# Performance work log

Hardware: AMD Instinct MI355X
Metric: run time of the kernel (lower is better)

## Reference

```python
import jax, jax.numpy as jnp
import numpy as np

B, S, D = 4, 2048, 1024
H, DK, DV = 16, 64, 64


def setup_inputs() -> dict:
    key = jax.random.key(0)
    kx, kq, kk, kv, ko = jax.random.split(key, 5)
    scale = 0.02
    return {
        "x": jax.random.normal(kx, (B, S, D), dtype=jnp.float32),
        "Wq": jax.random.normal(kq, (H, D, DK), dtype=jnp.float32) * scale,
        "Wk": jax.random.normal(kk, (H, D, DK), dtype=jnp.float32) * scale,
        "Wv": jax.random.normal(kv, (H, D, DV), dtype=jnp.float32) * scale,
        "Wo": jax.random.normal(ko, (H * DV, D), dtype=jnp.float32) * scale,
    }


def reference(x, Wq, Wk, Wv, Wo):
    # Per-head projections, batched over heads with einsum (same math as
    # the original per-head Linear loop).
    q = jnp.einsum("bsd,hdk->bhsk", x, Wq)  # [B,H,S,DK]
    k = jnp.einsum("bsd,hdk->bhsk", x, Wk)  # [B,H,S,DK]
    v = jnp.einsum("bsd,hdv->bhsv", x, Wv)  # [B,H,S,DV]

    scores = jnp.einsum("bhqk,bhsk->bhqs", q, k) / jnp.sqrt(
        jnp.asarray(DK, dtype=x.dtype)
    )  # [B,H,S,S]
    # Causal mask: position q attends only to s <= q.
    causal = jnp.tril(jnp.ones((S, S), dtype=bool))
    scores = jnp.where(causal, scores, jnp.asarray(-1e9, dtype=scores.dtype))
    attn = jax.nn.softmax(scores, axis=-1)

    ctx = jnp.einsum("bhqs,bhsv->bhqv", attn, v)  # [B,H,S,DV]
    # Concat heads: [B,S,H*DV], then output projection (no bias).
    ctx = ctx.transpose(0, 2, 1, 3).reshape(B, S, H * DV)
    return ctx @ Wo  # [B,S,D]
```

## Files before the change

### kernel.cpp

```cpp
#include <hip/hip_runtime.h>
#include <hip/hip_bf16.h>

#define SB 2048
#define DM 1024
#define NH 16
#define HD 64
#define BB 4
#define MTOT (BB * SB)
#define NW (DM * DM)
#define QSCALE 0.1803368801111244f

typedef __attribute__((ext_vector_type(8))) short bf16x8;
typedef __attribute__((ext_vector_type(4))) short bf16x4;
typedef __attribute__((ext_vector_type(4))) float f32x4;
typedef __attribute__((ext_vector_type(8))) __fp16 f16x8;
typedef __attribute__((ext_vector_type(4))) __fp16 f16x4;
typedef __attribute__((ext_vector_type(2))) __fp16 f16x2;

__device__ __forceinline__ short f2bf(float f) {
    union { float f; unsigned u; } a; a.f = f;
    unsigned r = (a.u + 0x7FFF + ((a.u >> 16) & 1)) >> 16;
    return (short)r;
}

__global__ __launch_bounds__(256) void cvt_all(const float* __restrict__ x,
                                               const float* __restrict__ Wq,
                                               const float* __restrict__ Wk,
                                               const float* __restrict__ Wv,
                                               const float* __restrict__ Wo,
                                               short* __restrict__ xb,
                                               short* __restrict__ wall,
                                               short* __restrict__ wot) {
    const int bid = blockIdx.x;
    const int t = threadIdx.x;
    if (bid < 4096) {
        const int i = (bid * 256 + t) * 8;
        float4 v0 = *(const float4*)(x + i);
        float4 v1 = *(const float4*)(x + i + 4);
        bf16x8 o = { f2bf(v0.x), f2bf(v0.y), f2bf(v0.z), f2bf(v0.w),
                     f2bf(v1.x), f2bf(v1.y), f2bf(v1.z), f2bf(v1.w) };
        *(bf16x8*)(xb + i) = o;
        return;
    }
    __shared__ float Ls[64][65];
    const int rem = bid - 4096;
    const int which = rem >> 8;
    const int rem2 = rem & 255;
    const float* in;
    short* out;
    int R, C;
    if (which < 3) {
        in = (which == 0) ? Wq : (which == 1) ? Wk : Wv;
        out = wall + (size_t)which * NW;
        R = DM; C = HD;
    } else {
        in = Wo; out = wot; R = DM; C = DM;
    }
    const int tilesC = C >> 6, tilesR = R >> 6;
    const int b = rem2 / (tilesR * tilesC);
    const int rr = rem2 % (tilesR * tilesC);
    const int R0 = (rr / tilesC) << 6;
    const int C0 = (rr % tilesC) << 6;
    const float* src = in + (size_t)b * R * C;
    short* dst = out + (size_t)b * R * C;
    const int r = t >> 2, c4 = (t & 3) << 4;
    const float* p = src + (size_t)(R0 + r) * C + C0 + c4;
#pragma unroll
    for (int u = 0; u < 16; u += 4) {
        float4 v = *(const float4*)(p + u);
        Ls[r][c4 + u] = v.x; Ls[r][c4 + u + 1] = v.y;
        Ls[r][c4 + u + 2] = v.z; Ls[r][c4 + u + 3] = v.w;
    }
    __syncthreads();
    const int cc = t >> 2, u2 = (t & 3) << 4;
    short* q = dst + (size_t)(C0 + cc) * R + R0 + u2;
    bf16x8 o0, o1;
#pragma unroll
    for (int j = 0; j < 8; ++j) o0[j] = f2bf(Ls[u2 + j][cc]);
#pragma unroll
    for (int j = 0; j < 8; ++j) o1[j] = f2bf(Ls[u2 + 8 + j][cc]);
    *(bf16x8*)(q) = o0;
    *(bf16x8*)(q + 8) = o1;
}

template <int MODE>
__global__ __launch_bounds__(256) void mm64(const short* __restrict__ A,
                                            const short* __restrict__ BT,
                                            short* __restrict__ qO,
                                            short* __restrict__ kO,
                                            _Float16* __restrict__ vO,
                                            float* __restrict__ fO) {
    __shared__ short sA[128 * 64];
    __shared__ short sB[128 * 64];
    const int t = threadIdx.x;
    const int lane = t & 63;
    const int w = t >> 6;
    const int wm = w >> 1, wn = w & 1;
    const int l15 = lane & 15, quad = lane >> 4;
    const int m0 = blockIdx.x * 128;
    const int n0 = blockIdx.y * 128;
    const bool isV = (MODE == 0) && (n0 >= 2048);

    f32x4 acc[4][4] = {};
    const int srow = t >> 3;
    const int schunk = t & 7;
    const int ssrc = ((schunk ^ (srow & 7)) << 3);
    const int sdst = (schunk << 3);
    const int r7 = l15 & 7;

    for (int k0 = 0; k0 < DM; k0 += 64) {
#pragma unroll
        for (int u = 0; u < 4; ++u) {
            const int row = u * 32 + srow;
            const short* ga = A + (size_t)(m0 + row) * DM + k0 + ssrc;
            const short* gb = BT + (size_t)(n0 + row) * DM + k0 + ssrc;
            __builtin_amdgcn_global_load_lds(
                (const __attribute__((address_space(1))) unsigned*)ga,
                (__attribute__((address_space(3))) unsigned*)&sA[(row << 6) + sdst],
                16, 0, 0);
            __builtin_amdgcn_global_load_lds(
                (const __attribute__((address_space(1))) unsigned*)gb,
                (__attribute__((address_space(3))) unsigned*)&sB[(row << 6) + sdst],
                16, 0, 0);
        }
        __syncthreads();

#pragma unroll
        for (int half = 0; half < 2; ++half) {
            bf16x8 af[4], bfr[4];
#pragma unroll
            for (int i = 0; i < 4; ++i) {
                const int ra = wm * 64 + i * 16 + l15;
                const int rb = wn * 64 + i * 16 + l15;
                const int ch = ((half * 4 + quad) ^ r7) << 3;
                af[i]  = *(const bf16x8*)&sA[(ra << 6) + ch];
                bfr[i] = *(const bf16x8*)&sB[(rb << 6) + ch];
            }
            if (isV) {
#pragma unroll
                for (int i = 0; i < 4; ++i)
#pragma unroll
                    for (int j = 0; j < 4; ++j)
                        acc[i][j] = __builtin_amdgcn_mfma_f32_16x16x32_bf16(af[i], bfr[j],
                                                                            acc[i][j], 0, 0, 0);
            } else {
#pragma unroll
                for (int i = 0; i < 4; ++i)
#pragma unroll
                    for (int j = 0; j < 4; ++j)
                        acc[i][j] = __builtin_amdgcn_mfma_f32_16x16x32_bf16(bfr[j], af[i],
                                                                            acc[i][j], 0, 0, 0);
            }
        }
        __syncthreads();
    }

    if (MODE == 1) {
#pragma unroll
        for (int i = 0; i < 4; ++i) {
            const int m = m0 + wm * 64 + i * 16 + l15;
#pragma unroll
            for (int j = 0; j < 4; ++j) {
                const int n = n0 + wn * 64 + j * 16 + quad * 4;
                f32x4 v = acc[i][j];
                *(float4*)&fO[(size_t)m * DM + n] = *(float4*)&v;
            }
        }
    } else if (isV) {
#pragma unroll
        for (int i = 0; i < 4; ++i) {
            const int m = m0 + wm * 64 + i * 16 + quad * 4;
            const int b = m >> 11, s0 = m & (SB - 1);
            const int sp = (s0 & ~31) | (((s0 >> 2) & 3) << 3) | (((s0 >> 4) & 1) << 2);
#pragma unroll
            for (int j = 0; j < 4; ++j) {
                const int nv = (n0 - 2048) + wn * 64 + j * 16 + l15;
                const int h = nv >> 6, d = nv & 63;
                f16x2 a = __builtin_amdgcn_cvt_pkrtz(acc[i][j][0], acc[i][j][1]);
                f16x2 b2 = __builtin_amdgcn_cvt_pkrtz(acc[i][j][2], acc[i][j][3]);
                f16x4 o = {a.x, a.y, b2.x, b2.y};
                *(f16x4*)&vO[((size_t)((b * NH + h) * HD + d)) * SB + sp] = o;
            }
        }
    } else {
#pragma unroll
        for (int i = 0; i < 4; ++i) {
            const int m = m0 + wm * 64 + i * 16 + l15;
            const int b = m >> 11, s = m & (SB - 1);
#pragma unroll
            for (int j = 0; j < 4; ++j) {
                const int n = n0 + wn * 64 + j * 16 + quad * 4;
                const int seg = n >> 10;
                const int h = (n & 1023) >> 6, d0 = n & 63;
                const float sc = (seg == 0) ? QSCALE : 1.0f;
                bf16x4 o;
#pragma unroll
                for (int r = 0; r < 4; ++r) o[r] = f2bf(acc[i][j][r] * sc);
                short* dst = (seg == 0) ? qO : kO;
                *(bf16x4*)&dst[(((size_t)(b * NH + h) * SB + s) << 6) + d0] = o;
            }
        }
    }
}

__global__ __launch_bounds__(256) void attn_mfma(const short* __restrict__ Q,
                                                 const short* __restrict__ K,
                                                 const _Float16* __restrict__ VT,
                                                 short* __restrict__ ctx) {
    __shared__ short    sK[2][64 * 64];
    __shared__ _Float16 sV[2][64 * 64];

    const int t = threadIdx.x;
    const int lane = t & 63, w = t >> 6;
    const int l15 = lane & 15, quad = lane >> 4;
    const int idx = blockIdx.x;
    const int bh = ((idx >> 7) << 3) | (idx & 7);
    const int pair = (idx >> 3) & 15;
    const int b = bh >> 4, h = bh & 15;
    const size_t hb = (size_t)bh * SB * HD;
    const short* Qb = Q + hb;
    const short* Kb = K + hb;
    const _Float16* Vb = VT + hb;

    const int srow = t >> 3;
    const int sch  = t & 7;
    const int srow2 = srow + 32;
    const int swl = l15 & 7;

    auto stage = [&](int k0, int bbuf) {
        __builtin_amdgcn_global_load_lds(
            (const __attribute__((address_space(1))) unsigned*)
                (Kb + (size_t)(k0 + srow) * HD + ((sch ^ (srow & 7)) << 3)),
            (__attribute__((address_space(3))) unsigned*)&sK[bbuf][t << 3], 16, 0, 0);
        __builtin_amdgcn_global_load_lds(
            (const __attribute__((address_space(1))) unsigned*)
                (Kb + (size_t)(k0 + srow2) * HD + ((sch ^ (srow2 & 7)) << 3)),
            (__attribute__((address_space(3))) unsigned*)&sK[bbuf][(t + 256) << 3], 16, 0, 0);
        __builtin_amdgcn_global_load_lds(
            (const __attribute__((address_space(1))) unsigned*)
                (Vb + (size_t)srow * SB + k0 + ((sch ^ (srow & 7)) << 3)),
            (__attribute__((address_space(3))) unsigned*)&sV[bbuf][t << 3], 16, 0, 0);
        __builtin_amdgcn_global_load_lds(
            (const __attribute__((address_space(1))) unsigned*)
                (Vb + (size_t)srow2 * SB + k0 + ((sch ^ (srow2 & 7)) << 3)),
            (__attribute__((address_space(3))) unsigned*)&sV[bbuf][(t + 256) << 3], 16, 0, 0);
    };

#pragma unroll
    for (int ph = 0; ph < 2; ++ph) {
        const int qt = ph ? (31 - pair) : pair;
        const int qw = qt * 64 + w * 16;

        bf16x8 aq[2];
#pragma unroll
        for (int hh = 0; hh < 2; ++hh)
            aq[hh] = *(const bf16x8*)(Qb + (size_t)(qw + l15) * HD + hh * 32 + quad * 8);

        f32x4 O[4] = {};
        float l_r = 0.f;

        __syncthreads();
        stage(0, 0);

#pragma unroll 2
        for (int kt = 0; kt <= qt; ++kt) {
            __syncthreads();
            if (kt < qt) stage((kt + 1) * 64, (kt + 1) & 1);

            const int buf = kt & 1;
            const bool diag = (kt == qt);
            const short* sKb = &sK[buf][0];
            const _Float16* sVb = &sV[buf][0];

            f32x4 sc[4] = {};
#pragma unroll
            for (int st = 0; st < 4; ++st) {
                const int row = st * 16 + l15;
#pragma unroll
                for (int hh = 0; hh < 2; ++hh) {
                    bf16x8 kf = *(const bf16x8*)&sKb[(row << 6) +
                                                     (((hh * 4 + quad) ^ swl) << 3)];
                    sc[st] = __builtin_amdgcn_mfma_f32_16x16x32_bf16(kf, aq[hh], sc[st], 0, 0, 0);
                }
            }

#pragma unroll
            for (int stp = 0; stp < 2; ++stp) {
                if (diag && stp * 2 > w) break;
                f16x8 vv[4];
                const int vch = ((stp * 4 + quad) ^ swl) << 3;
#pragma unroll
                for (int dj = 0; dj < 4; ++dj)
                    vv[dj] = *(const f16x8*)&sVb[((dj * 16 + l15) << 6) + vch];
#pragma unroll
                for (int half = 0; half < 2; ++half) {
                    const int st = stp * 2 + half;
                    if (diag && st > w) break;
                    float p[4];
                    if (!diag || st < w) {
#pragma unroll
                        for (int r = 0; r < 4; ++r) p[r] = __builtin_amdgcn_exp2f(sc[st][r]);
                    } else {
#pragma unroll
                        for (int r = 0; r < 4; ++r)
                            p[r] = (quad * 4 + r <= l15) ? __builtin_amdgcn_exp2f(sc[st][r]) : 0.f;
                    }
                    l_r += (p[0] + p[1]) + (p[2] + p[3]);
                    f16x2 pa = __builtin_amdgcn_cvt_pkrtz(p[0], p[1]);
                    f16x2 pb = __builtin_amdgcn_cvt_pkrtz(p[2], p[3]);
                    f16x4 pf = {pa.x, pa.y, pb.x, pb.y};
#pragma unroll
                    for (int dj = 0; dj < 4; ++dj) {
                        f16x4 vfh;
                        if (half == 0)
                            vfh = __builtin_shufflevector(vv[dj], vv[dj], 0, 1, 2, 3);
                        else
                            vfh = __builtin_shufflevector(vv[dj], vv[dj], 4, 5, 6, 7);
                        O[dj] = __builtin_amdgcn_mfma_f32_16x16x16f16(vfh, pf, O[dj], 0, 0, 0);
                    }
                }
            }
        }

        float l = l_r;
        l += __shfl_xor(l, 16);
        l += __shfl_xor(l, 32);
        const float inv = 1.f / l;
        const int q = qw + l15;
#pragma unroll
        for (int dj = 0; dj < 4; ++dj) {
            bf16x4 o;
#pragma unroll
            for (int r = 0; r < 4; ++r) o[r] = f2bf(O[dj][r] * inv);
            *(bf16x4*)&ctx[(size_t)(b * SB + q) * DM + h * HD + dj * 16 + quad * 4] = o;
        }
    }
}

extern "C" void kernel_launch(void* const* d_in, const int* in_sizes, int n_in,
                              void* d_out, int out_size, void* d_ws, size_t ws_size,
                              hipStream_t stream) {
    const float* x  = (const float*)d_in[0];
    const float* Wq = (const float*)d_in[1];
    const float* Wk = (const float*)d_in[2];
    const float* Wv = (const float*)d_in[3];
    const float* Wo = (const float*)d_in[4];
    float* out = (float*)d_out;

    const size_t NX = (size_t)MTOT * DM;
    short* xb   = (short*)d_ws;
    short* wall = xb + NX;
    short* wot  = wall + 3 * (size_t)NW;
    short* qb   = wot + NW;
    short* kb   = qb + NX;
    short* vtb  = kb + NX;
    short* ctxb = vtb + NX;

    dim3 blk(256);
    cvt_all<<<4096 + 1024, blk, 0, stream>>>(x, Wq, Wk, Wv, Wo, xb, wall, wot);

    dim3 gqkv(MTOT / 128, 3072 / 128);
    mm64<0><<<gqkv, blk, 0, stream>>>(xb, wall, qb, kb, (_Float16*)vtb, nullptr);

    attn_mfma<<<dim3(1024), blk, 0, stream>>>(qb, kb, (const _Float16*)vtb, ctxb);

    dim3 gout(MTOT / 128, DM / 128);
    mm64<1><<<gout, blk, 0, stream>>>(ctxb, wot, nullptr, nullptr, nullptr, out);
}
```

Baseline: 243.3 us.

## Give each attention wave two query groups and shrink the out-projection tile

The attention kernel drops from 256 to 128 threads per block, and each wave now handles 32 query rows as two 16-row groups. Each K/V fragment read from shared memory therefore feeds twice as many MFMAs, which cuts LDS traffic per unit of work. The output projection moves to a dedicated 64x128-tile kernel, doubling the block count for better occupancy and load balance on the small output GEMM. The costs are higher register pressure in attention from doubled accumulators and fewer waves per block to hide latency.

```diff
diff --git a/kernel.cpp b/kernel.cpp
--- a/kernel.cpp
+++ b/kernel.cpp
@@ -83,13 +83,11 @@
     *(bf16x8*)(q + 8) = o1;
 }
 
-template <int MODE>
-__global__ __launch_bounds__(256) void mm64(const short* __restrict__ A,
-                                            const short* __restrict__ BT,
-                                            short* __restrict__ qO,
-                                            short* __restrict__ kO,
-                                            _Float16* __restrict__ vO,
-                                            float* __restrict__ fO) {
+__global__ __launch_bounds__(256) void mm_qkv(const short* __restrict__ A,
+                                              const short* __restrict__ BT,
+                                              short* __restrict__ qO,
+                                              short* __restrict__ kO,
+                                              _Float16* __restrict__ vO) {
     __shared__ short sA[128 * 64];
     __shared__ short sB[128 * 64];
     const int t = threadIdx.x;
@@ -99,7 +97,7 @@
     const int l15 = lane & 15, quad = lane >> 4;
     const int m0 = blockIdx.x * 128;
     const int n0 = blockIdx.y * 128;
-    const bool isV = (MODE == 0) && (n0 >= 2048);
+    const bool isV = (n0 >= 2048);
 
     f32x4 acc[4][4] = {};
     const int srow = t >> 3;
@@ -155,18 +153,7 @@
         __syncthreads();
     }
 
-    if (MODE == 1) {
-#pragma unroll
-        for (int i = 0; i < 4; ++i) {
-            const int m = m0 + wm * 64 + i * 16 + l15;
-#pragma unroll
-            for (int j = 0; j < 4; ++j) {
-                const int n = n0 + wn * 64 + j * 16 + quad * 4;
-                f32x4 v = acc[i][j];
-                *(float4*)&fO[(size_t)m * DM + n] = *(float4*)&v;
-            }
-        }
-    } else if (isV) {
+    if (isV) {
 #pragma unroll
         for (int i = 0; i < 4; ++i) {
             const int m = m0 + wm * 64 + i * 16 + quad * 4;
@@ -203,7 +190,77 @@
     }
 }
 
-__global__ __launch_bounds__(256) void attn_mfma(const short* __restrict__ Q,
+__global__ __launch_bounds__(256) void mm_out64(const short* __restrict__ A,
+                                                const short* __restrict__ BT,
+                                                float* __restrict__ fO) {
+    __shared__ short sA[64 * 64];
+    __shared__ short sB[128 * 64];
+    const int t = threadIdx.x;
+    const int lane = t & 63;
+    const int w = t >> 6;
+    const int l15 = lane & 15, quad = lane >> 4;
+    const int m0 = blockIdx.x * 64;
+    const int n0 = blockIdx.y * 128;
+
+    f32x4 acc[4][2] = {};
+    const int r7 = l15 & 7;
+
+    for (int k0 = 0; k0 < DM; k0 += 64) {
+#pragma unroll
+        for (int u = 0; u < 2; ++u) {
+            const int f = t + 256 * u;
+            const int row = f >> 3;
+            const int ch = ((f & 7) ^ (row & 7)) << 3;
+            __builtin_amdgcn_global_load_lds(
+                (const __attribute__((address_space(1))) unsigned*)
+                    (A + (size_t)(m0 + row) * DM + k0 + ch),
+                (__attribute__((address_space(3))) unsigned*)&sA[f << 3], 16, 0, 0);
+        }
+#pragma unroll
+        for (int u = 0; u < 4; ++u) {
+            const int f = t + 256 * u;
+            const int row = f >> 3;
+            const int ch = ((f & 7) ^ (row & 7)) << 3;
+            __builtin_amdgcn_global_load_lds(
+                (const __attribute__((address_space(1))) unsigned*)
+                    (BT + (size_t)(n0 + row) * DM + k0 + ch),
+                (__attribute__((address_space(3))) unsigned*)&sB[f << 3], 16, 0, 0);
+        }
+        __syncthreads();
+
+#pragma unroll
+        for (int half = 0; half < 2; ++half) {
+            const int ch = ((half * 4 + quad) ^ r7) << 3;
+            bf16x8 af[4], bfr[2];
+#pragma unroll
+            for (int i = 0; i < 4; ++i)
+                af[i] = *(const bf16x8*)&sA[((i * 16 + l15) << 6) + ch];
+#pragma unroll
+            for (int j = 0; j < 2; ++j)
+                bfr[j] = *(const bf16x8*)&sB[((w * 32 + j * 16 + l15) << 6) + ch];
+#pragma unroll
+            for (int i = 0; i < 4; ++i)
+#pragma unroll
+                for (int j = 0; j < 2; ++j)
+                    acc[i][j] = __builtin_amdgcn_mfma_f32_16x16x32_bf16(bfr[j], af[i],
+                                                                        acc[i][j], 0, 0, 0);
+        }
+        __syncthreads();
+    }
+
+#pragma unroll
+    for (int i = 0; i < 4; ++i) {
+        const int m = m0 + i * 16 + l15;
+#pragma unroll
+        for (int j = 0; j < 2; ++j) {
+            const int n = n0 + w * 32 + j * 16 + quad * 4;
+            f32x4 v = acc[i][j];
+            *(float4*)&fO[(size_t)m * DM + n] = *(float4*)&v;
+        }
+    }
+}
+
+__global__ __launch_bounds__(128) void attn_mfma(const short* __restrict__ Q,
                                                  const short* __restrict__ K,
                                                  const _Float16* __restrict__ VT,
                                                  short* __restrict__ ctx) {
@@ -222,47 +279,44 @@
     const short* Kb = K + hb;
     const _Float16* Vb = VT + hb;
 
-    const int srow = t >> 3;
-    const int sch  = t & 7;
-    const int srow2 = srow + 32;
     const int swl = l15 & 7;
 
     auto stage = [&](int k0, int bbuf) {
-        __builtin_amdgcn_global_load_lds(
-            (const __attribute__((address_space(1))) unsigned*)
-                (Kb + (size_t)(k0 + srow) * HD + ((sch ^ (srow & 7)) << 3)),
-            (__attribute__((address_space(3))) unsigned*)&sK[bbuf][t << 3], 16, 0, 0);
-        __builtin_amdgcn_global_load_lds(
-            (const __attribute__((address_space(1))) unsigned*)
-                (Kb + (size_t)(k0 + srow2) * HD + ((sch ^ (srow2 & 7)) << 3)),
-            (__attribute__((address_space(3))) unsigned*)&sK[bbuf][(t + 256) << 3], 16, 0, 0);
-        __builtin_amdgcn_global_load_lds(
-            (const __attribute__((address_space(1))) unsigned*)
-                (Vb + (size_t)srow * SB + k0 + ((sch ^ (srow & 7)) << 3)),
-            (__attribute__((address_space(3))) unsigned*)&sV[bbuf][t << 3], 16, 0, 0);
-        __builtin_amdgcn_global_load_lds(
-            (const __attribute__((address_space(1))) unsigned*)
-                (Vb + (size_t)srow2 * SB + k0 + ((sch ^ (srow2 & 7)) << 3)),
-            (__attribute__((address_space(3))) unsigned*)&sV[bbuf][(t + 256) << 3], 16, 0, 0);
+#pragma unroll
+        for (int u = 0; u < 4; ++u) {
+            const int f = t + 128 * u;
+            const int row = f >> 3;
+            const int ch = ((f & 7) ^ (row & 7)) << 3;
+            __builtin_amdgcn_global_load_lds(
+                (const __attribute__((address_space(1))) unsigned*)
+                    (Kb + (size_t)(k0 + row) * HD + ch),
+                (__attribute__((address_space(3))) unsigned*)&sK[bbuf][f << 3], 16, 0, 0);
+            __builtin_amdgcn_global_load_lds(
+                (const __attribute__((address_space(1))) unsigned*)
+                    (Vb + (size_t)row * SB + k0 + ch),
+                (__attribute__((address_space(3))) unsigned*)&sV[bbuf][f << 3], 16, 0, 0);
+        }
     };
 
 #pragma unroll
     for (int ph = 0; ph < 2; ++ph) {
         const int qt = ph ? (31 - pair) : pair;
-        const int qw = qt * 64 + w * 16;
-
-        bf16x8 aq[2];
-#pragma unroll
-        for (int hh = 0; hh < 2; ++hh)
-            aq[hh] = *(const bf16x8*)(Qb + (size_t)(qw + l15) * HD + hh * 32 + quad * 8);
-
-        f32x4 O[4] = {};
-        float l_r = 0.f;
+        const int qw = qt * 64 + w * 32;
+
+        bf16x8 aq[2][2];
+#pragma unroll
+        for (int qg = 0; qg < 2; ++qg)
+#pragma unroll
+            for (int hh = 0; hh < 2; ++hh)
+                aq[qg][hh] = *(const bf16x8*)(Qb + (size_t)(qw + qg * 16 + l15) * HD +
+                                              hh * 32 + quad * 8);
+
+        f32x4 O[2][4] = {};
+        float l_r[2] = {0.f, 0.f};
 
         __syncthreads();
         stage(0, 0);
 
-#pragma unroll 2
         for (int kt = 0; kt <= qt; ++kt) {
             __syncthreads();
             if (kt < qt) stage((kt + 1) * 64, (kt + 1) & 1);
@@ -272,7 +326,7 @@
             const short* sKb = &sK[buf][0];
             const _Float16* sVb = &sV[buf][0];
 
-            f32x4 sc[4] = {};
+            f32x4 sc[2][4] = {};
 #pragma unroll
             for (int st = 0; st < 4; ++st) {
                 const int row = st * 16 + l15;
@@ -280,13 +334,14 @@
                 for (int hh = 0; hh < 2; ++hh) {
                     bf16x8 kf = *(const bf16x8*)&sKb[(row << 6) +
                                                      (((hh * 4 + quad) ^ swl) << 3)];
-                    sc[st] = __builtin_amdgcn_mfma_f32_16x16x32_bf16(kf, aq[hh], sc[st], 0, 0, 0);
+                    sc[0][st] = __builtin_amdgcn_mfma_f32_16x16x32_bf16(kf, aq[0][hh], sc[0][st], 0, 0, 0);
+                    sc[1][st] = __builtin_amdgcn_mfma_f32_16x16x32_bf16(kf, aq[1][hh], sc[1][st], 0, 0, 0);
                 }
             }
 
 #pragma unroll
             for (int stp = 0; stp < 2; ++stp) {
-                if (diag && stp * 2 > w) break;
+                if (diag && stp * 2 > 2 * w + 1) break;
                 f16x8 vv[4];
                 const int vch = ((stp * 4 + quad) ^ swl) << 3;
 #pragma unroll
@@ -295,44 +350,54 @@
 #pragma unroll
                 for (int half = 0; half < 2; ++half) {
                     const int st = stp * 2 + half;
-                    if (diag && st > w) break;
-                    float p[4];
-                    if (!diag || st < w) {
-#pragma unroll
-                        for (int r = 0; r < 4; ++r) p[r] = __builtin_amdgcn_exp2f(sc[st][r]);
-                    } else {
-#pragma unroll
-                        for (int r = 0; r < 4; ++r)
-                            p[r] = (quad * 4 + r <= l15) ? __builtin_amdgcn_exp2f(sc[st][r]) : 0.f;
-                    }
-                    l_r += (p[0] + p[1]) + (p[2] + p[3]);
-                    f16x2 pa = __builtin_amdgcn_cvt_pkrtz(p[0], p[1]);
-                    f16x2 pb = __builtin_amdgcn_cvt_pkrtz(p[2], p[3]);
-                    f16x4 pf = {pa.x, pa.y, pb.x, pb.y};
-#pragma unroll
-                    for (int dj = 0; dj < 4; ++dj) {
-                        f16x4 vfh;
-                        if (half == 0)
-                            vfh = __builtin_shufflevector(vv[dj], vv[dj], 0, 1, 2, 3);
-                        else
-                            vfh = __builtin_shufflevector(vv[dj], vv[dj], 4, 5, 6, 7);
-                        O[dj] = __builtin_amdgcn_mfma_f32_16x16x16f16(vfh, pf, O[dj], 0, 0, 0);
+#pragma unroll
+                    for (int qg = 0; qg < 2; ++qg) {
+                        const int dloc = 2 * w + qg;
+                        if (diag && st > dloc) continue;
+                        float p[4];
+                        if (!diag || st < dloc) {
+#pragma unroll
+                            for (int r = 0; r < 4; ++r)
+                                p[r] = __builtin_amdgcn_exp2f(sc[qg][st][r]);
+                        } else {
+#pragma unroll
+                            for (int r = 0; r < 4; ++r)
+                                p[r] = (quad * 4 + r <= l15)
+                                           ? __builtin_amdgcn_exp2f(sc[qg][st][r]) : 0.f;
+                        }
+                        l_r[qg] += (p[0] + p[1]) + (p[2] + p[3]);
+                        f16x2 pa = __builtin_amdgcn_cvt_pkrtz(p[0], p[1]);
+                        f16x2 pb = __builtin_amdgcn_cvt_pkrtz(p[2], p[3]);
+                        f16x4 pf = {pa.x, pa.y, pb.x, pb.y};
+#pragma unroll
+                        for (int dj = 0; dj < 4; ++dj) {
+                            f16x4 vfh;
+                            if (half == 0)
+                                vfh = __builtin_shufflevector(vv[dj], vv[dj], 0, 1, 2, 3);
+                            else
+                                vfh = __builtin_shufflevector(vv[dj], vv[dj], 4, 5, 6, 7);
+                            O[qg][dj] = __builtin_amdgcn_mfma_f32_16x16x16f16(vfh, pf,
+                                                                              O[qg][dj], 0, 0, 0);
+                        }
                     }
                 }
             }
         }
 
-        float l = l_r;
-        l += __shfl_xor(l, 16);
-        l += __shfl_xor(l, 32);
-        const float inv = 1.f / l;
-        const int q = qw + l15;
-#pragma unroll
-        for (int dj = 0; dj < 4; ++dj) {
-            bf16x4 o;
-#pragma unroll
-            for (int r = 0; r < 4; ++r) o[r] = f2bf(O[dj][r] * inv);
-            *(bf16x4*)&ctx[(size_t)(b * SB + q) * DM + h * HD + dj * 16 + quad * 4] = o;
+#pragma unroll
+        for (int qg = 0; qg < 2; ++qg) {
+            float l = l_r[qg];
+            l += __shfl_xor(l, 16);
+            l += __shfl_xor(l, 32);
+            const float inv = 1.f / l;
+            const int q = qw + qg * 16 + l15;
+#pragma unroll
+            for (int dj = 0; dj < 4; ++dj) {
+                bf16x4 o;
+#pragma unroll
+                for (int r = 0; r < 4; ++r) o[r] = f2bf(O[qg][dj][r] * inv);
+                *(bf16x4*)&ctx[(size_t)(b * SB + q) * DM + h * HD + dj * 16 + quad * 4] = o;
+            }
         }
     }
 }
@@ -360,10 +425,10 @@
     cvt_all<<<4096 + 1024, blk, 0, stream>>>(x, Wq, Wk, Wv, Wo, xb, wall, wot);
 
     dim3 gqkv(MTOT / 128, 3072 / 128);
-    mm64<0><<<gqkv, blk, 0, stream>>>(xb, wall, qb, kb, (_Float16*)vtb, nullptr);
-
-    attn_mfma<<<dim3(1024), blk, 0, stream>>>(qb, kb, (const _Float16*)vtb, ctxb);
-
-    dim3 gout(MTOT / 128, DM / 128);
-    mm64<1><<<gout, blk, 0, stream>>>(ctxb, wot, nullptr, nullptr, nullptr, out);
-}
+    mm_qkv<<<gqkv, blk, 0, stream>>>(xb, wall, qb, kb, (_Float16*)vtb);
+
+    attn_mfma<<<dim3(1024), dim3(128), 0, stream>>>(qb, kb, (const _Float16*)vtb, ctxb);
+
+    dim3 gout(MTOT / 64, DM / 128);
+    mm_out64<<<gout, blk, 0, stream>>>(ctxb, wot, out);
+}
```

After: 255.6 us. 1.05x slower.
